# Kernel optimization log

Measured on AMD Instinct MI355X. Metric: run time of the kernel, lower is better.

The kernel has to match this reference:

```python
import jax, jax.numpy as jnp
from jax import lax
import numpy as np

B, S, D_IN, D_OUT, LAT, N_STATE = 8, 2048, 1024, 1024, 256, 32
D_INNER, D_CONV, DT_RANK, N_BLK = 2 * D_OUT, 4, D_OUT // 16, 2


def setup_inputs() -> dict:
    key = jax.random.key(0)
    ks = iter(jax.random.split(key, 24))
    r = lambda shp, s=0.02: jax.random.normal(next(ks), shp, dtype=jnp.float32) * s
    inp = {
        "x": jax.random.normal(next(ks), (B, S, D_IN), dtype=jnp.float32),
        "W_in": r((D_IN, D_OUT)), "b_in": jnp.zeros((D_OUT,), jnp.float32),
        "Wa1": r((D_OUT, LAT)), "ba1": jnp.zeros((LAT,), jnp.float32),
        "Wa2": r((LAT, LAT)), "ba2": jnp.zeros((LAT,), jnp.float32),
        # per-block params, leading axis = N_BLK
        "gamma": jnp.ones((N_BLK, D_OUT), jnp.float32),
        "in_proj_w": r((N_BLK, D_OUT, 2 * D_INNER)),
        "conv_w": r((N_BLK, D_INNER, D_CONV), 0.1),
        "conv_b": jnp.zeros((N_BLK, D_INNER), jnp.float32),
        "x_proj_w": r((N_BLK, D_INNER, DT_RANK + 2 * N_STATE)),
        "dt_proj_w": r((N_BLK, DT_RANK, D_INNER), 0.1),
        "dt_proj_b": jnp.full((N_BLK, D_INNER), -4.6, jnp.float32),  # softplus(-4.6)~0.01
        "A_log": jnp.log(jnp.broadcast_to(jnp.arange(1, N_STATE + 1, dtype=jnp.float32), (N_BLK, D_INNER, N_STATE))),
        "D": jnp.ones((N_BLK, D_INNER), jnp.float32),
        "out_proj_w": r((N_BLK, D_INNER, D_OUT)),
    }
    return inp


def rms_norm(x, gamma):
    # F.normalize(x, dim=-1) * sqrt(d) * gamma
    norm = jnp.sqrt(jnp.sum(x * x, axis=-1, keepdims=True))
    return x / jnp.maximum(norm, 1e-12) * (x.shape[-1] ** 0.5) * gamma


def causal_conv1d(x, w, b):
    # x: [b, d, L], w: [d, d_conv] depthwise, causal (left) padding
    y = lax.conv_general_dilated(
        x, w[:, None, :], window_strides=(1,), padding=[(D_CONV - 1, 0)],
        feature_group_count=x.shape[1], dimension_numbers=("NCH", "OIH", "NCH"))
    return y + b[None, :, None]


def selective_scan(dA, dBu, C):
    # dA, dBu: [b, L, d_inner, n], C: [b, L, n] -> y: [b, L, d_inner]
    def step(h, inp):
        dA_t, dBu_t, C_t = inp
        h = dA_t * h + dBu_t
        return h, jnp.einsum("bdn,bn->bd", h, C_t)
    h0 = jnp.zeros(dA.shape[:1] + dA.shape[2:], dA.dtype)
    _, ys = lax.scan(step, h0, (dA.swapaxes(0, 1), dBu.swapaxes(0, 1), C.swapaxes(0, 1)))
    return ys.swapaxes(0, 1)


def mamba(u, in_w, cw, cb, xw, dtw, dtb, A_log, Dp, ow):
    # u: [b, L, d_model]
    xz = u @ in_w                              # [b, L, 2*d_inner]
    xh, z = jnp.split(xz, 2, axis=-1)
    xh = causal_conv1d(xh.swapaxes(1, 2), cw, cb).swapaxes(1, 2)
    xh = jax.nn.silu(xh)                       # [b, L, d_inner]
    xdbc = xh @ xw                             # [b, L, dt_rank + 2n]
    dt, Bm, Cm = jnp.split(xdbc, [DT_RANK, DT_RANK + N_STATE], axis=-1)
    dt = jax.nn.softplus(dt @ dtw + dtb)       # [b, L, d_inner]
    A = -jnp.exp(A_log)                        # [d_inner, n]
    dA = jnp.exp(dt[..., None] * A)            # [b, L, d_inner, n]
    dBu = dt[..., None] * Bm[:, :, None, :] * xh[..., None]
    y = selective_scan(dA, dBu, Cm) + Dp * xh
    y = y * jax.nn.silu(z)
    return y @ ow


def reference(x, W_in, b_in, Wa1, ba1, Wa2, ba2, gamma, in_proj_w, conv_w,
              conv_b, x_proj_w, dt_proj_w, dt_proj_b, A_log, D, out_proj_w):
    out = x @ W_in + b_in                      # [b, s, d]
    length = out.shape[1]
    w = jax.nn.silu(out @ Wa1 + ba1) @ Wa2 + ba2   # [b, s, LAT]
    w1 = jax.nn.softmax(w, axis=-1) * (LAT / length)
    w2 = jax.nn.softmax(w, axis=-2)
    weights = (w1 + w2) * 0.5
    out = jnp.einsum("bsd,bsS->bSd", out, weights)  # [b, LAT, d]
    for i in range(N_BLK):  # residual RMSNorm + Mamba (dropout = identity in eval)
        out = out + mamba(rms_norm(out, gamma[i]), in_proj_w[i], conv_w[i],
                          conv_b[i], x_proj_w[i], dt_proj_w[i], dt_proj_b[i],
                          A_log[i], D[i], out_proj_w[i])
    return out
```

## Files before the change

### kernel.cpp

```cpp
#include <hip/hip_runtime.h>
#include <math.h>
#include <stdint.h>

#define BB 8
#define SS 2048
#define D_IN 1024
#define D_OUTC 1024
#define LATC 256
#define NSTATE 32
#define DINNER 2048
#define DCONV 4
#define DTRANK 64
#define NCH 32

__device__ __forceinline__ float silu_f(float v) { return v * (1.f / (1.f + __expf(-v))); }
__device__ __forceinline__ float softplus_f(float v) {
    return fmaxf(v, 0.f) + log1pf(__expf(-fabsf(v)));
}

typedef short short8 __attribute__((ext_vector_type(8)));
typedef float f32x4 __attribute__((ext_vector_type(4)));

__device__ __forceinline__ unsigned short f2bf(float f) {
    unsigned u = __builtin_bit_cast(unsigned, f);
    u += 0x7FFFu + ((u >> 16) & 1u);
    return (unsigned short)(u >> 16);
}
__device__ __forceinline__ int pack2(float a, float b) {
    return (int)((unsigned)f2bf(a) | ((unsigned)f2bf(b) << 16));
}

typedef const __attribute__((address_space(1))) unsigned int* gas_ptr;
typedef __attribute__((address_space(3))) unsigned int* las_ptr;
__device__ __forceinline__ void gload16(const void* g, void* l) {
    __builtin_amdgcn_global_load_lds(
        reinterpret_cast<gas_ptr>(reinterpret_cast<uintptr_t>(g)),
        reinterpret_cast<las_ptr>(reinterpret_cast<uintptr_t>(l)),
        16, 0, 0);
}

__global__ __launch_bounds__(256) void transp_bf(const float* __restrict__ src,
                                                 unsigned short* __restrict__ dst,
                                                 int K, int N)
{
    __shared__ float tile[32][33];
    const int n0 = blockIdx.x * 32;
    const int k0 = blockIdx.y * 32;
    const int x = threadIdx.x & 31;
    const int y = threadIdx.x >> 5;
#pragma unroll
    for (int j = 0; j < 4; j++)
        tile[y + 8 * j][x] = src[(size_t)(k0 + y + 8 * j) * N + n0 + x];
    __syncthreads();
#pragma unroll
    for (int j = 0; j < 4; j++)
        dst[(size_t)(n0 + y + 8 * j) * K + k0 + x] = f2bf(tile[x][y + 8 * j]);
}

__global__ __launch_bounds__(256) void cvt_bf16(const float* __restrict__ in,
                                                unsigned short* __restrict__ out)
{
    size_t i = ((size_t)blockIdx.x * 256 + threadIdx.x) * 8;
    float4 a = *(const float4*)(in + i);
    float4 b = *(const float4*)(in + i + 4);
    int4 w;
    w.x = pack2(a.x, a.y); w.y = pack2(a.z, a.w);
    w.z = pack2(b.x, b.y); w.w = pack2(b.z, b.w);
    *(int4*)(out + i) = w;
}

__global__ __launch_bounds__(256) void gemm16(
    const unsigned short* __restrict__ A, int lda,
    const unsigned short* __restrict__ BT, int ldb,
    const float* __restrict__ bias,
    float* __restrict__ C, int ldc,
    unsigned short* __restrict__ C16, int ldc16,
    int M, int N, int K, int act, int accum)
{
    __shared__ __align__(16) unsigned short As[128 * 32];
    __shared__ __align__(16) unsigned short Bs[128 * 32];

    const int tid = threadIdx.x;
    const int lane = tid & 63;
    const int wave = tid >> 6;
    const int wr = wave >> 1;
    const int wc = wave & 1;
    const int quad = lane >> 4;
    const int l16 = lane & 15;

    const int m0 = blockIdx.y * 128;
    const int n0 = blockIdx.x * 128;

    const int srow4 = lane >> 2;
    const int sphys = lane & 3;

    f32x4 acc[4][4];
#pragma unroll
    for (int i = 0; i < 4; i++)
#pragma unroll
        for (int j = 0; j < 4; j++) acc[i][j] = (f32x4){0.f, 0.f, 0.f, 0.f};

    for (int k0 = 0; k0 < K; k0 += 32) {
#pragma unroll
        for (int i = 0; i < 2; i++) {
            const int rr = (wave << 5) + (i << 4) + srow4;
            const int ls = sphys ^ ((rr >> 1) & 3);
            unsigned short* ldsA = &As[((wave << 5) + (i << 4)) << 5];
            unsigned short* ldsB = &Bs[((wave << 5) + (i << 4)) << 5];
            gload16(A + (size_t)(m0 + rr) * lda + (k0 + (ls << 3)), ldsA);
            gload16(BT + (size_t)(n0 + rr) * ldb + (k0 + (ls << 3)), ldsB);
        }
        __syncthreads();

        short8 af[4], bfr[4];
#pragma unroll
        for (int i = 0; i < 4; i++) {
            const int ar = (wr << 6) + (i << 4) + l16;
            af[i] = *(const short8*)&As[(ar << 5) + ((quad ^ ((ar >> 1) & 3)) << 3)];
            const int br = (wc << 6) + (i << 4) + l16;
            bfr[i] = *(const short8*)&Bs[(br << 5) + ((quad ^ ((br >> 1) & 3)) << 3)];
        }
#pragma unroll
        for (int i = 0; i < 4; i++)
#pragma unroll
            for (int j = 0; j < 4; j++)
                acc[i][j] = __builtin_amdgcn_mfma_f32_16x16x32_bf16(af[i], bfr[j], acc[i][j], 0, 0, 0);
        __syncthreads();
    }

#pragma unroll
    for (int j = 0; j < 4; j++) {
        int gn = n0 + wc * 64 + j * 16 + l16;
        float bv = bias ? bias[gn] : 0.f;
#pragma unroll
        for (int i = 0; i < 4; i++) {
#pragma unroll
            for (int r = 0; r < 4; r++) {
                int gm = m0 + wr * 64 + i * 16 + quad * 4 + r;
                float v = acc[i][j][r] + bv;
                if (act == 1) v = silu_f(v);
                else if (act == 2) v = softplus_f(v);
                if (C) {
                    size_t ci = (size_t)gm * ldc + gn;
                    if (accum) C[ci] += v;
                    else C[ci] = v;
                }
                if (C16) C16[(size_t)gm * ldc16 + gn] = f2bf(v);
            }
        }
    }
}

__global__ __launch_bounds__(256) void gemm_mix(
    const float* __restrict__ A, int lda, long strideA,
    const unsigned short* __restrict__ B16, int ldb, long strideB,
    float* __restrict__ C, int ldc, long strideC,
    int M, int N, int K)
{
    __shared__ __align__(16) unsigned short As[128][40];
    __shared__ __align__(16) unsigned short Bs[128][40];

    const int bz = blockIdx.z;
    const float* Ab = A + (size_t)bz * strideA;
    const unsigned short* Bb = B16 + (size_t)bz * strideB;
    float* Cb = C + (size_t)bz * strideC;

    const int tid = threadIdx.x;
    const int lane = tid & 63;
    const int wave = tid >> 6;
    const int wr = wave >> 1;
    const int wc = wave & 1;
    const int quad = lane >> 4;
    const int l16 = lane & 15;

    const int m0 = blockIdx.y * 128;
    const int n0 = blockIdx.x * 128;

    f32x4 acc[4][4];
#pragma unroll
    for (int i = 0; i < 4; i++)
#pragma unroll
        for (int j = 0; j < 4; j++) acc[i][j] = (f32x4){0.f, 0.f, 0.f, 0.f};

    for (int k0 = 0; k0 < K; k0 += 32) {
        {
            int kr = tid >> 3;
            int x0 = (tid & 7) * 16;
            const float* src = Ab + (size_t)(k0 + kr) * lda + (m0 + x0);
#pragma unroll
            for (int q = 0; q < 4; q++) {
                float4 f = *(const float4*)(src + q * 4);
                As[x0 + q * 4 + 0][kr] = f2bf(f.x);
                As[x0 + q * 4 + 1][kr] = f2bf(f.y);
                As[x0 + q * 4 + 2][kr] = f2bf(f.z);
                As[x0 + q * 4 + 3][kr] = f2bf(f.w);
            }
        }
        {
            int kr = tid >> 3;
            int x0 = (tid & 7) * 16;
            const unsigned short* src = Bb + (size_t)(k0 + kr) * ldb + (n0 + x0);
            short8 v0 = *(const short8*)(src);
            short8 v1 = *(const short8*)(src + 8);
#pragma unroll
            for (int q = 0; q < 8; q++) Bs[x0 + q][kr] = (unsigned short)v0[q];
#pragma unroll
            for (int q = 0; q < 8; q++) Bs[x0 + 8 + q][kr] = (unsigned short)v1[q];
        }
        __syncthreads();

        short8 af[4], bfr[4];
#pragma unroll
        for (int i = 0; i < 4; i++) {
            af[i] = *(const short8*)&As[wr * 64 + i * 16 + l16][quad * 8];
            bfr[i] = *(const short8*)&Bs[wc * 64 + i * 16 + l16][quad * 8];
        }
#pragma unroll
        for (int i = 0; i < 4; i++)
#pragma unroll
            for (int j = 0; j < 4; j++)
                acc[i][j] = __builtin_amdgcn_mfma_f32_16x16x32_bf16(af[i], bfr[j], acc[i][j], 0, 0, 0);
        __syncthreads();
    }

#pragma unroll
    for (int j = 0; j < 4; j++) {
        int gn = n0 + wc * 64 + j * 16 + l16;
#pragma unroll
        for (int i = 0; i < 4; i++) {
#pragma unroll
            for (int r = 0; r < 4; r++) {
                int gm = m0 + wr * 64 + i * 16 + quad * 4 + r;
                Cb[(size_t)gm * ldc + gn] = acc[i][j][r];
            }
        }
    }
}

__global__ __launch_bounds__(256) void gemm_kernel(
    const float* __restrict__ A, int lda, long strideA,
    const float* __restrict__ B, int ldb, long strideB,
    const float* __restrict__ bias,
    float* __restrict__ C, int ldc, long strideC,
    int M, int N, int K, int transA, int act, int accum)
{
    __shared__ float As[16][65];
    __shared__ float Bsh[16][64];

    const int bz = blockIdx.z;
    const float* Ab = A + (size_t)bz * strideA;
    const float* Bb = B + (size_t)bz * strideB;
    float* Cb = C + (size_t)bz * strideC;

    const int tx = threadIdx.x;
    const int ty = threadIdx.y;
    const int tid = ty * 16 + tx;
    const int m0 = blockIdx.y * 64;
    const int n0 = blockIdx.x * 64;

    float acc[4][4];
#pragma unroll
    for (int i = 0; i < 4; i++)
#pragma unroll
        for (int j = 0; j < 4; j++) acc[i][j] = 0.f;

    for (int k0 = 0; k0 < K; k0 += 16) {
        if (!transA) {
            int row = tid >> 2;
            int kc = (tid & 3) * 4;
            int gm = m0 + row;
#pragma unroll
            for (int j = 0; j < 4; j++) {
                int gk = k0 + kc + j;
                As[kc + j][row] = (gm < M && gk < K) ? Ab[(size_t)gm * lda + gk] : 0.f;
            }
        } else {
            int krow = tid >> 4;
            int mc = (tid & 15) * 4;
            int gk = k0 + krow;
#pragma unroll
            for (int j = 0; j < 4; j++) {
                int gm = m0 + mc + j;
                As[krow][mc + j] = (gm < M && gk < K) ? Ab[(size_t)gk * lda + gm] : 0.f;
            }
        }
        {
            int krow = tid >> 4;
            int nc = (tid & 15) * 4;
            int gk = k0 + krow;
#pragma unroll
            for (int j = 0; j < 4; j++) {
                int gn = n0 + nc + j;
                Bsh[krow][nc + j] = (gk < K && gn < N) ? Bb[(size_t)gk * ldb + gn] : 0.f;
            }
        }
        __syncthreads();
#pragma unroll
        for (int k = 0; k < 16; k++) {
            float a[4], bv[4];
#pragma unroll
            for (int i = 0; i < 4; i++) a[i] = As[k][ty * 4 + i];
#pragma unroll
            for (int j = 0; j < 4; j++) bv[j] = Bsh[k][tx * 4 + j];
#pragma unroll
            for (int i = 0; i < 4; i++)
#pragma unroll
                for (int j = 0; j < 4; j++) acc[i][j] += a[i] * bv[j];
        }
        __syncthreads();
    }

#pragma unroll
    for (int i = 0; i < 4; i++) {
        int gm = m0 + ty * 4 + i;
        if (gm >= M) continue;
#pragma unroll
        for (int j = 0; j < 4; j++) {
            int gn = n0 + tx * 4 + j;
            if (gn >= N) continue;
            float v = acc[i][j];
            if (bias) v += bias[gn];
            if (act == 1) v = silu_f(v);
            else if (act == 2) v = softplus_f(v);
            size_t ci = (size_t)gm * ldc + gn;
            if (accum) Cb[ci] += v;
            else Cb[ci] = v;
        }
    }
}

__global__ __launch_bounds__(256) void merge4_kernel(const float* __restrict__ part,
                                                     float* __restrict__ out, int n)
{
    int i = blockIdx.x * 256 + threadIdx.x;
    out[i] = part[i] + part[i + n] + part[i + 2 * n] + part[i + 3 * n];
}

__global__ __launch_bounds__(256) void colstats_part_kernel(const float* __restrict__ w,
                                                            float* __restrict__ part)
{
    int b = blockIdx.x / NCH;
    int ch = blockIdx.x % NCH;
    int l = threadIdx.x;
    const float* base = w + ((size_t)b * SS + (size_t)ch * (SS / NCH)) * LATC + l;
    float m = -1e30f, s = 0.f;
    for (int t = 0; t < SS / NCH; t++) {
        float v = base[(size_t)t * LATC];
        float nm = fmaxf(m, v);
        s = s * __expf(m - nm) + __expf(v - nm);
        m = nm;
    }
    float2* p = (float2*)part;
    p[(size_t)(b * LATC + l) * NCH + ch] = make_float2(m, s);
}

__global__ __launch_bounds__(256) void colstats_merge_kernel(const float* __restrict__ part,
                                                             float* __restrict__ colst)
{
    int idx = blockIdx.x * 256 + threadIdx.x;
    const float2* p = (const float2*)part + (size_t)idx * NCH;
    float m = -1e30f, s = 0.f;
#pragma unroll 4
    for (int c = 0; c < NCH; c++) {
        float2 v = p[c];
        float nm = fmaxf(m, v.x);
        s = s * __expf(m - nm) + v.y * __expf(v.x - nm);
        m = nm;
    }
    colst[idx * 2] = m;
    colst[idx * 2 + 1] = s;
}

__global__ __launch_bounds__(256) void softmix_kernel(float* __restrict__ w,
                                                      const float* __restrict__ colst)
{
    int bs = blockIdx.x;
    int b = bs / SS;
    int l = threadIdx.x;
    float* row = w + (size_t)bs * LATC;
    float v = row[l];

    __shared__ float sm[256];
    sm[l] = v;
    __syncthreads();
    for (int st = 128; st > 0; st >>= 1) {
        if (l < st) sm[l] = fmaxf(sm[l], sm[l + st]);
        __syncthreads();
    }
    float rmax = sm[0];
    __syncthreads();
    float e = __expf(v - rmax);
    sm[l] = e;
    __syncthreads();
    for (int st = 128; st > 0; st >>= 1) {
        if (l < st) sm[l] += sm[l + st];
        __syncthreads();
    }
    float rsum = sm[0];

    float w1 = e / rsum * ((float)LATC / (float)SS);
    float cm = colst[(b * LATC + l) * 2];
    float cs = colst[(b * LATC + l) * 2 + 1];
    float w2 = __expf(v - cm) / cs;
    row[l] = 0.5f * (w1 + w2);
}

__global__ __launch_bounds__(256) void rmsnorm_kernel(const float* __restrict__ x,
                                                      const float* __restrict__ gamma,
                                                      unsigned short* __restrict__ out)
{
    int row = blockIdx.x;
    const float* xr = x + (size_t)row * D_OUTC;
    float v[4];
    float ss = 0.f;
#pragma unroll
    for (int i = 0; i < 4; i++) {
        v[i] = xr[threadIdx.x + i * 256];
        ss += v[i] * v[i];
    }
#pragma unroll
    for (int off = 32; off >= 1; off >>= 1) ss += __shfl_xor(ss, off, 64);
    __shared__ float sred[4];
    int wave = threadIdx.x >> 6;
    if ((threadIdx.x & 63) == 0) sred[wave] = ss;
    __syncthreads();
    float tot = sred[0] + sred[1] + sred[2] + sred[3];
    float inv = 32.0f / fmaxf(sqrtf(tot), 1e-12f);
    unsigned short* outr = out + (size_t)row * D_OUTC;
#pragma unroll
    for (int i = 0; i < 4; i++) {
        int d = threadIdx.x + i * 256;
        outr[d] = f2bf(v[i] * inv * gamma[d]);
    }
}

__global__ __launch_bounds__(256) void conv_silu_kernel(const float* __restrict__ xz,
                                                        const float* __restrict__ cw,
                                                        const float* __restrict__ cb,
                                                        float* __restrict__ xh, int L)
{
    int idx = blockIdx.x * 256 + threadIdx.x;
    int c = idx % DINNER;
    int bl = idx / DINNER;
    int l = bl % L;
    int b = bl / L;
    float acc = cb[c];
#pragma unroll
    for (int j = 0; j < DCONV; j++) {
        int ls = l - (DCONV - 1) + j;
        if (ls >= 0)
            acc += xz[((size_t)(b * L + ls)) * (2 * DINNER) + c] * cw[c * DCONV + j];
    }
    xh[idx] = silu_f(acc);
}

#define SCH 4
__global__ __launch_bounds__(256) void scan_kernel(const float* __restrict__ dty,
                                                   const float* __restrict__ xh,
                                                   const float* __restrict__ xz,
                                                   const float* __restrict__ xdbc,
                                                   const float* __restrict__ A_log,
                                                   const float* __restrict__ Dp,
                                                   unsigned short* __restrict__ ybf,
                                                   int L)
{
    const int t = threadIdx.x;
    const int g = t & 7;
    const int dloc = t >> 3;
    const int b = blockIdx.x >> 6;
    const int d = ((blockIdx.x & 63) << 5) + dloc;

    float4 Av = *(const float4*)(A_log + (size_t)d * NSTATE + g * 4);
    const float A0 = -__expf(Av.x), A1 = -__expf(Av.y), A2 = -__expf(Av.z), A3 = -__expf(Av.w);
    float h0 = 0.f, h1 = 0.f, h2 = 0.f, h3 = 0.f;
    const float Dd = Dp[d];

    const float* pdt = dty + (size_t)b * L * DINNER + d;
    const float* pxh = xh + (size_t)b * L * DINNER + d;
    const float* pz  = xz + (size_t)b * L * 2 * DINNER + DINNER + d;
    const float* pbc = xdbc + (size_t)b * L * 128 + DTRANK + g * 4;
    unsigned short* pout = ybf + (size_t)b * L * DINNER + d;

    float a_dt[SCH], a_x[SCH], a_z[SCH];
    float4 a_B[SCH], a_C[SCH];
    float n_dt[SCH], n_x[SCH], n_z[SCH];
    float4 n_B[SCH], n_C[SCH];

#pragma unroll
    for (int j = 0; j < SCH; j++) {
        a_dt[j] = pdt[(size_t)j * DINNER];
        a_x[j]  = pxh[(size_t)j * DINNER];
        a_z[j]  = pz[(size_t)j * 2 * DINNER];
        a_B[j]  = *(const float4*)(pbc + (size_t)j * 128);
        a_C[j]  = *(const float4*)(pbc + (size_t)j * 128 + NSTATE);
    }

    for (int l0 = 0; l0 < L; l0 += SCH) {
        const int lb = (l0 + SCH < L) ? (l0 + SCH) : l0;
#pragma unroll
        for (int j = 0; j < SCH; j++) {
            n_dt[j] = pdt[(size_t)(lb + j) * DINNER];
            n_x[j]  = pxh[(size_t)(lb + j) * DINNER];
            n_z[j]  = pz[(size_t)(lb + j) * 2 * DINNER];
            n_B[j]  = *(const float4*)(pbc + (size_t)(lb + j) * 128);
            n_C[j]  = *(const float4*)(pbc + (size_t)(lb + j) * 128 + NSTATE);
        }
#pragma unroll
        for (int j = 0; j < SCH; j++) {
            float dtv = a_dt[j], xv = a_x[j], zv = a_z[j];
            float dtx = dtv * xv;
            float e0 = __expf(dtv * A0);
            float e1 = __expf(dtv * A1);
            float e2 = __expf(dtv * A2);
            float e3 = __expf(dtv * A3);
            h0 = e0 * h0 + dtx * a_B[j].x;
            h1 = e1 * h1 + dtx * a_B[j].y;
            h2 = e2 * h2 + dtx * a_B[j].z;
            h3 = e3 * h3 + dtx * a_B[j].w;
            float accv = h0 * a_C[j].x + h1 * a_C[j].y + h2 * a_C[j].z + h3 * a_C[j].w;
            accv += __shfl_xor(accv, 1, 64);
            accv += __shfl_xor(accv, 2, 64);
            accv += __shfl_xor(accv, 4, 64);
            if (g == 0) {
                float yv = (accv + Dd * xv) * silu_f(zv);
                pout[(size_t)(l0 + j) * DINNER] = f2bf(yv);
            }
        }
#pragma unroll
        for (int j = 0; j < SCH; j++) {
            a_dt[j] = n_dt[j]; a_x[j] = n_x[j]; a_z[j] = n_z[j];
            a_B[j] = n_B[j];   a_C[j] = n_C[j];
        }
    }
}


extern "C" void kernel_launch(void* const* d_in, const int* in_sizes, int n_in,
                              void* d_out, int out_size, void* d_ws, size_t ws_size,
                              hipStream_t stream)
{
    const float* x      = (const float*)d_in[0];
    const float* W_in   = (const float*)d_in[1];
    const float* b_in   = (const float*)d_in[2];
    const float* Wa1    = (const float*)d_in[3];
    const float* ba1    = (const float*)d_in[4];
    const float* Wa2    = (const float*)d_in[5];
    const float* ba2    = (const float*)d_in[6];
    const float* gamma  = (const float*)d_in[7];
    const float* in_w   = (const float*)d_in[8];
    const float* conv_w = (const float*)d_in[9];
    const float* conv_b = (const float*)d_in[10];
    const float* x_w    = (const float*)d_in[11];
    const float* dt_w   = (const float*)d_in[12];
    const float* dt_b   = (const float*)d_in[13];
    const float* A_log  = (const float*)d_in[14];
    const float* Dp     = (const float*)d_in[15];
    const float* out_w  = (const float*)d_in[16];
    float* latout = (float*)d_out;

    char* wsb = (char*)d_ws;
    const size_t MB = 1 << 20;

    unsigned short* out0_bf = (unsigned short*)(wsb);
    unsigned short* xbf     = (unsigned short*)(wsb + 32 * MB);
    float*          wbuf    = (float*)(wsb + 64 * MB);
    unsigned short* t1_bf   = (unsigned short*)(wsb + 80 * MB);
    unsigned short* WinT    = (unsigned short*)(wsb + 88 * MB);
    unsigned short* Wa1T    = (unsigned short*)(wsb + 90 * MB);
    unsigned short* Wa2T    = (unsigned short*)(wsb + 90 * MB + 512 * 1024);
    float*          cs_part = (float*)(wsb + 91 * MB);
    float*          colst   = (float*)(wsb + 95 * MB);

    unsigned short* unorm_bf  = (unsigned short*)(wsb);
    float*          xdbc_part = (float*)(wsb + 4 * MB);
    float*          dtbuf     = (float*)(wsb + 8 * MB);
    unsigned short* ybf       = (unsigned short*)(wsb + 24 * MB);
    float*          xz        = (float*)(wsb + 32 * MB);
    float*          xh        = (float*)(wsb + 64 * MB);
    unsigned short* wprojT    = (unsigned short*)(wsb + 80 * MB);
    unsigned short* oprojT    = (unsigned short*)(wsb + 88 * MB);
    float*          xdbc      = (float*)(wsb + 92 * MB);

    dim3 blk(16, 16);
    const int L = LATC;
    const int M1 = BB * SS;
    const int ML = BB * L;

    cvt_bf16<<<dim3((size_t)M1 * D_IN / 2048), dim3(256), 0, stream>>>(x, xbf);
    transp_bf<<<dim3(D_OUTC / 32, D_IN / 32), dim3(256), 0, stream>>>(W_in, WinT, D_IN, D_OUTC);
    transp_bf<<<dim3(LATC / 32, D_OUTC / 32), dim3(256), 0, stream>>>(Wa1, Wa1T, D_OUTC, LATC);
    transp_bf<<<dim3(LATC / 32, LATC / 32), dim3(256), 0, stream>>>(Wa2, Wa2T, LATC, LATC);

    gemm16<<<dim3(D_OUTC / 128, M1 / 128), dim3(256), 0, stream>>>(
        xbf, D_IN, WinT, D_IN, b_in, (float*)nullptr, 0, out0_bf, D_OUTC,
        M1, D_OUTC, D_IN, 0, 0);

    gemm16<<<dim3(LATC / 128, M1 / 128), dim3(256), 0, stream>>>(
        out0_bf, D_OUTC, Wa1T, D_OUTC, ba1, (float*)nullptr, 0, t1_bf, LATC,
        M1, LATC, D_OUTC, 1, 0);

    gemm16<<<dim3(LATC / 128, M1 / 128), dim3(256), 0, stream>>>(
        t1_bf, LATC, Wa2T, LATC, ba2, wbuf, LATC, (unsigned short*)nullptr, 0,
        M1, LATC, LATC, 0, 0);

    colstats_part_kernel<<<dim3(BB * NCH), dim3(256), 0, stream>>>(wbuf, cs_part);
    colstats_merge_kernel<<<dim3(BB * LATC / 256), dim3(256), 0, stream>>>(cs_part, colst);
    softmix_kernel<<<dim3(BB * SS), dim3(256), 0, stream>>>(wbuf, colst);

    gemm_mix<<<dim3(D_OUTC / 128, LATC / 128, BB), dim3(256), 0, stream>>>(
        wbuf, LATC, (long)SS * LATC, out0_bf, D_OUTC, (long)SS * D_OUTC,
        latout, D_OUTC, (long)LATC * D_OUTC, LATC, D_OUTC, SS);

    for (int i = 0; i < 2; i++) {
        const float* in_wi = in_w + (size_t)i * D_OUTC * 2 * DINNER;
        const float* cwi = conv_w + (size_t)i * DINNER * DCONV;
        const float* cbi = conv_b + (size_t)i * DINNER;
        const float* xwi = x_w + (size_t)i * DINNER * (DTRANK + 2 * NSTATE);
        const float* dtwi = dt_w + (size_t)i * DTRANK * DINNER;
        const float* dtbi = dt_b + (size_t)i * DINNER;
        const float* Ali = A_log + (size_t)i * DINNER * NSTATE;
        const float* Dpi = Dp + (size_t)i * DINNER;
        const float* owi = out_w + (size_t)i * DINNER * D_OUTC;
        const float* gi = gamma + (size_t)i * D_OUTC;

        transp_bf<<<dim3(2 * DINNER / 32, D_OUTC / 32), dim3(256), 0, stream>>>(
            in_wi, wprojT, D_OUTC, 2 * DINNER);
        transp_bf<<<dim3(D_OUTC / 32, DINNER / 32), dim3(256), 0, stream>>>(
            owi, oprojT, DINNER, D_OUTC);

        rmsnorm_kernel<<<dim3(ML), dim3(256), 0, stream>>>(latout, gi, unorm_bf);

        gemm16<<<dim3(2 * DINNER / 128, ML / 128), dim3(256), 0, stream>>>(
            unorm_bf, D_OUTC, wprojT, D_OUTC, (const float*)nullptr,
            xz, 2 * DINNER, (unsigned short*)nullptr, 0,
            ML, 2 * DINNER, D_OUTC, 0, 0);

        conv_silu_kernel<<<dim3(BB * L * DINNER / 256), dim3(256), 0, stream>>>(xz, cwi, cbi, xh, L);

        gemm_kernel<<<dim3(128 / 64, ML / 64, 4), blk, 0, stream>>>(
            xh, DINNER, 512, xwi, 128, (long)512 * 128, (const float*)nullptr,
            xdbc_part, 128, (long)ML * 128, ML, 128, 512, 0, 0, 0);
        merge4_kernel<<<dim3(ML * 128 / 256), dim3(256), 0, stream>>>(
            xdbc_part, xdbc, ML * 128);

        gemm_kernel<<<dim3(DINNER / 64, ML / 64, 1), blk, 0, stream>>>(
            xdbc, 128, 0, dtwi, DINNER, 0, dtbi, dtbuf, DINNER, 0, ML, DINNER, DTRANK, 0, 2, 0);

        scan_kernel<<<dim3(BB * DINNER * 8 / 256), dim3(256), 0, stream>>>(
            dtbuf, xh, xz, xdbc, Ali, Dpi, ybf, L);

        gemm16<<<dim3(D_OUTC / 128, ML / 128), dim3(256), 0, stream>>>(
            ybf, DINNER, oprojT, DINNER, (const float*)nullptr,
            latout, D_OUTC, (unsigned short*)nullptr, 0,
            ML, D_OUTC, DINNER, 0, 1);
    }
}
```

Measured before the change: 1.087 ms.

## Double-buffer LDS tiles in bf16 GEMM and swizzle workgroups across XCDs

The bf16 MFMA GEMM now uses two LDS buffers, so the global-to-LDS loads for the next K-tile are issued before the MFMAs on the current tile. This overlaps memory latency with compute and removes one barrier per iteration. It also remaps block IDs so consecutive tiles are grouped per XCD, which is meant to improve L2 reuse on MI355X. The cost is doubled LDS use (32KB), which may reduce occupancy.

```diff
diff --git a/kernel.cpp b/kernel.cpp
--- a/kernel.cpp
+++ b/kernel.cpp
@@ -77,8 +77,8 @@
     unsigned short* __restrict__ C16, int ldc16,
     int M, int N, int K, int act, int accum)
 {
-    __shared__ __align__(16) unsigned short As[128 * 32];
-    __shared__ __align__(16) unsigned short Bs[128 * 32];
+    __shared__ __align__(16) unsigned short As[2][128 * 32];
+    __shared__ __align__(16) unsigned short Bs[2][128 * 32];
 
     const int tid = threadIdx.x;
     const int lane = tid & 63;
@@ -88,8 +88,15 @@
     const int quad = lane >> 4;
     const int l16 = lane & 15;
 
-    const int m0 = blockIdx.y * 128;
-    const int n0 = blockIdx.x * 128;
+    const int nbx = gridDim.x;
+    const int nwg = nbx * gridDim.y;
+    const int orig = blockIdx.y * nbx + blockIdx.x;
+    const int q = nwg >> 3, r = nwg & 7;
+    const int xcd = orig & 7, lid = orig >> 3;
+    const int swz = (xcd < r) ? (xcd * (q + 1) + lid)
+                              : (r * (q + 1) + (xcd - r) * q + lid);
+    const int m0 = (swz / nbx) * 128;
+    const int n0 = (swz % nbx) * 128;
 
     const int srow4 = lane >> 2;
     const int sphys = lane & 3;
@@ -100,32 +107,45 @@
 #pragma unroll
         for (int j = 0; j < 4; j++) acc[i][j] = (f32x4){0.f, 0.f, 0.f, 0.f};
 
-    for (int k0 = 0; k0 < K; k0 += 32) {
+    const int nt = K >> 5;
+
+    auto STAGE = [&](int buf, int t) {
+        const int k0 = t << 5;
 #pragma unroll
         for (int i = 0; i < 2; i++) {
-            const int rr = (wave << 5) + (i << 4) + srow4;
+            const int rbase = (wave << 5) + (i << 4);
+            const int rr = rbase + srow4;
             const int ls = sphys ^ ((rr >> 1) & 3);
-            unsigned short* ldsA = &As[((wave << 5) + (i << 4)) << 5];
-            unsigned short* ldsB = &Bs[((wave << 5) + (i << 4)) << 5];
-            gload16(A + (size_t)(m0 + rr) * lda + (k0 + (ls << 3)), ldsA);
-            gload16(BT + (size_t)(n0 + rr) * ldb + (k0 + (ls << 3)), ldsB);
-        }
-        __syncthreads();
+            gload16(A + (size_t)(m0 + rr) * lda + (k0 + (ls << 3)), &As[buf][rbase << 5]);
+            gload16(BT + (size_t)(n0 + rr) * ldb + (k0 + (ls << 3)), &Bs[buf][rbase << 5]);
+        }
+    };
+
+    STAGE(0, 0);
+    asm volatile("s_waitcnt vmcnt(0)" ::: "memory");
+    __syncthreads();
+
+    int cur = 0;
+    for (int t = 0; t < nt; ++t) {
+        if (t + 1 < nt) STAGE(cur ^ 1, t + 1);
 
         short8 af[4], bfr[4];
 #pragma unroll
         for (int i = 0; i < 4; i++) {
             const int ar = (wr << 6) + (i << 4) + l16;
-            af[i] = *(const short8*)&As[(ar << 5) + ((quad ^ ((ar >> 1) & 3)) << 3)];
+            af[i] = *(const short8*)&As[cur][(ar << 5) + ((quad ^ ((ar >> 1) & 3)) << 3)];
             const int br = (wc << 6) + (i << 4) + l16;
-            bfr[i] = *(const short8*)&Bs[(br << 5) + ((quad ^ ((br >> 1) & 3)) << 3)];
+            bfr[i] = *(const short8*)&Bs[cur][(br << 5) + ((quad ^ ((br >> 1) & 3)) << 3)];
         }
 #pragma unroll
         for (int i = 0; i < 4; i++)
 #pragma unroll
             for (int j = 0; j < 4; j++)
                 acc[i][j] = __builtin_amdgcn_mfma_f32_16x16x32_bf16(af[i], bfr[j], acc[i][j], 0, 0, 0);
+
+        asm volatile("s_waitcnt vmcnt(0)" ::: "memory");
         __syncthreads();
+        cur ^= 1;
     }
 
 #pragma unroll
@@ -135,9 +155,9 @@
 #pragma unroll
         for (int i = 0; i < 4; i++) {
 #pragma unroll
-            for (int r = 0; r < 4; r++) {
-                int gm = m0 + wr * 64 + i * 16 + quad * 4 + r;
-                float v = acc[i][j][r] + bv;
+            for (int r2 = 0; r2 < 4; r2++) {
+                int gm = m0 + wr * 64 + i * 16 + quad * 4 + r2;
+                float v = acc[i][j][r2] + bv;
                 if (act == 1) v = silu_f(v);
                 else if (act == 2) v = softplus_f(v);
                 if (C) {
```

New measurement: 1.033 ms. 5.0% less time.
